# Kernel optimization log

Measured on AMD Instinct MI355X. Metric: run time of the kernel, lower is better.

Reference implementation:

```python
import jax, jax.numpy as jnp
import numpy as np

D_LATENT = 128   # per-head dim AND input embedding dim (d_q default)
N_HEADS = 16
ROPE_BASE = 10000.0


def _rope(x):
    # x: [B, H, S, D]; interleaved-pair rotary embedding over seq axis (-2)
    B, H, S, D = x.shape
    half = D // 2
    inv_freq = 1.0 / (ROPE_BASE ** (jnp.arange(half, dtype=jnp.float32) * 2.0 / D))
    ang = jnp.arange(S, dtype=jnp.float32)[:, None] * inv_freq[None, :]  # [S, half]
    cos, sin = jnp.cos(ang), jnp.sin(ang)
    xp = x.reshape(B, H, S, half, 2)
    x0, x1 = xp[..., 0], xp[..., 1]
    r0 = x0 * cos - x1 * sin
    r1 = x1 * cos + x0 * sin
    return jnp.stack([r0, r1], axis=-1).reshape(B, H, S, D)


def setup_inputs() -> dict:
    key = jax.random.key(0)
    k_q, k_wq, k_wk, k_wv, k_wo = jax.random.split(key, 5)
    B, S, E = 2, 2048, D_LATENT
    inner = N_HEADS * D_LATENT
    sc_in = 1.0 / np.sqrt(E)
    sc_inner = 1.0 / np.sqrt(inner)
    return {
        "q": jax.random.normal(k_q, (B, S, E), dtype=jnp.float32),
        "W_q": jax.random.normal(k_wq, (E, inner), dtype=jnp.float32) * sc_in,
        "W_k": jax.random.normal(k_wk, (E, inner), dtype=jnp.float32) * sc_in,
        "W_v": jax.random.normal(k_wv, (E, inner), dtype=jnp.float32) * sc_in,
        "W_o": jax.random.normal(k_wo, (inner, E), dtype=jnp.float32) * sc_inner,
    }


def reference(q, W_q, W_k, W_v, W_o):
    B, S, E = q.shape
    H, D = N_HEADS, D_LATENT
    scale = 1.0 / np.sqrt(D)
    # projections -> [B, H, S, D]
    qh = (q @ W_q).reshape(B, S, H, D).transpose(0, 2, 1, 3)
    kh = (q @ W_k).reshape(B, S, H, D).transpose(0, 2, 1, 3)
    vh = (q @ W_v).reshape(B, S, H, D).transpose(0, 2, 1, 3)
    qh = _rope(qh)
    kh = _rope(kh)
    scores = jnp.einsum("bhsd,bhtd->bhst", qh, kh) * scale  # [B,H,S,S]
    causal = jnp.tril(jnp.ones((S, S), dtype=bool))
    scores = jnp.where(causal, scores, -jnp.inf)
    probs = jax.nn.softmax(scores, axis=-1)
    out = jnp.einsum("bhst,bhtd->bhsd", probs, vh)  # [B,H,S,D]
    out = out.transpose(0, 2, 1, 3).reshape(B, S, H * D)
    return out @ W_o
```

## Files before the change

kernel.cpp:

```cpp
#include <hip/hip_runtime.h>
#include <math.h>

#define S_LEN 2048
#define NH 16
#define DH 128
#define INNER 2048
#define NROWS 4096

typedef __attribute__((ext_vector_type(8))) short bf16x8;
typedef __attribute__((ext_vector_type(4))) float f32x4;

__device__ __forceinline__ short f2bf(float f) {
  union { float f; unsigned u; } v; v.f = f;
  unsigned r = (v.u + 0x7fffu + ((v.u >> 16) & 1u)) >> 16;
  return (short)(unsigned short)r;
}
__device__ __forceinline__ float bf2f(short s) {
  union { unsigned u; float f; } v; v.u = ((unsigned)(unsigned short)s) << 16;
  return v.f;
}
__device__ __forceinline__ void gl2lds(const short* g, short* l) {
  __builtin_amdgcn_global_load_lds(
      (const __attribute__((address_space(1))) unsigned int*)g,
      (__attribute__((address_space(3))) unsigned int*)l, 16, 0, 0);
}

__global__ void k_prep(const float* __restrict__ X, const float* __restrict__ Wq,
                       const float* __restrict__ Wk, const float* __restrict__ Wv,
                       const float* __restrict__ Wo,
                       float* __restrict__ rcT, float* __restrict__ rsT,
                       short* __restrict__ Xbf, short* __restrict__ WT,
                       short* __restrict__ WoT) {
  const int bx = blockIdx.x, tid = threadIdx.x;
  if (bx < 512) {
    int idx = bx * 256 + tid;
    int i = idx >> 11, s = idx & 2047;
    double invf = pow(10000.0, -(double)i / 64.0);
    float ang = (float)((double)s * invf);
    float sv, cv; sincosf(ang, &sv, &cv);
    rcT[idx] = cv; rsT[idx] = sv;
    return;
  }
  if (bx < 1024) {
    int idx = ((bx - 512) * 256 + tid) * 4;
    float4 xv = *(const float4*)&X[idx];
    short4 o; o.x = f2bf(xv.x); o.y = f2bf(xv.y); o.z = f2bf(xv.z); o.w = f2bf(xv.w);
    *(short4*)&Xbf[idx] = o;
    return;
  }
  __shared__ float tile[32][33];
  const float* src; short* dst; int R, C, c0, r0;
  if (bx < 1792) {
    int z = (bx - 1024) >> 8, t = (bx - 1024) & 255;
    src = (z == 0) ? Wq : ((z == 1) ? Wk : Wv);
    dst = WT + (size_t)z * INNER * 128; R = 128; C = INNER;
    c0 = (t & 63) * 32; r0 = (t >> 6) * 32;
  } else {
    int t = bx - 1792;
    src = Wo; dst = WoT; R = INNER; C = 128;
    c0 = (t & 3) * 32; r0 = (t >> 2) * 32;
  }
  int tx = tid & 31, ty = tid >> 5;
  #pragma unroll
  for (int dy = 0; dy < 32; dy += 8)
    tile[ty + dy][tx] = src[(size_t)(r0 + ty + dy) * C + c0 + tx];
  __syncthreads();
  #pragma unroll
  for (int dy = 0; dy < 32; dy += 8)
    dst[(size_t)(c0 + ty + dy) * R + r0 + tx] = f2bf(tile[tx][ty + dy]);
}

__global__ __launch_bounds__(256, 2) void k_qkv(
    const short* __restrict__ Xbf, const short* __restrict__ WT,
    const float* __restrict__ rcT, const float* __restrict__ rsT,
    short* __restrict__ Qg, short* __restrict__ Kg, short* __restrict__ Vg) {
  __shared__ __attribute__((aligned(16))) short As[128 * 136];
  __shared__ __attribute__((aligned(16))) short Bs[128 * 136];
  const int tid = threadIdx.x;
  const int n0 = blockIdx.x * 128, m0 = blockIdx.y * 128;
  for (int e = tid; e < 2048; e += 256)
    *(int4*)&As[(e >> 4) * 136 + (e & 15) * 8] =
        *(const int4*)&Xbf[(size_t)(m0 + (e >> 4)) * 128 + (e & 15) * 8];
  const int wid = tid >> 6, lane = tid & 63;
  const int l16 = lane & 15, quad = lane >> 4;
  const int wm = (wid & 1) * 64, wn = (wid >> 1) * 64;
  const int hh = n0 >> 7;
  const int bb = m0 >> 11, ss = m0 & 2047;
  const float qscale = 0.08838834764831845f;
  for (int z = 0; z < 3; ++z) {
    __syncthreads();
    const short* Wp = WT + (size_t)z * INNER * 128;
    for (int e = tid; e < 2048; e += 256)
      *(int4*)&Bs[(e >> 4) * 136 + (e & 15) * 8] =
          *(const int4*)&Wp[(size_t)(n0 + (e >> 4)) * 128 + (e & 15) * 8];
    __syncthreads();
    f32x4 acc[4][4] = {};
    #pragma unroll
    for (int ks = 0; ks < 4; ++ks) {
      bf16x8 a[4], b[4];
      #pragma unroll
      for (int mt = 0; mt < 4; ++mt)
        a[mt] = *(const bf16x8*)&As[(wm + mt * 16 + l16) * 136 + ks * 32 + quad * 8];
      #pragma unroll
      for (int nt = 0; nt < 4; ++nt)
        b[nt] = *(const bf16x8*)&Bs[(wn + nt * 16 + l16) * 136 + ks * 32 + quad * 8];
      #pragma unroll
      for (int mt = 0; mt < 4; ++mt)
        #pragma unroll
        for (int nt = 0; nt < 4; ++nt)
          acc[mt][nt] = __builtin_amdgcn_mfma_f32_16x16x32_bf16(a[mt], b[nt], acc[mt][nt], 0, 0, 0);
    }
    if (z < 2) {
      __syncthreads();
      #pragma unroll
      for (int mt = 0; mt < 4; ++mt)
        #pragma unroll
        for (int nt = 0; nt < 4; ++nt) {
          int d = wn + nt * 16 + l16, i = d >> 1;
          int sl0 = wm + mt * 16 + quad * 4;
          float4 c4 = *(const float4*)&rcT[i * S_LEN + ss + sl0];
          float4 s4 = *(const float4*)&rsT[i * S_LEN + ss + sl0];
          float cA[4] = {c4.x, c4.y, c4.z, c4.w};
          float sA[4] = {s4.x, s4.y, s4.z, s4.w};
          #pragma unroll
          for (int r = 0; r < 4; ++r) {
            float v = acc[mt][nt][r];
            float pv = __shfl_xor(v, 1);
            float res = (d & 1) ? (v * cA[r] + pv * sA[r]) : (v * cA[r] - pv * sA[r]);
            if (z == 0) res *= qscale;
            Bs[(sl0 + r) * 136 + d] = f2bf(res);
          }
        }
      __syncthreads();
      short* dst = (z == 0 ? Qg : Kg) + (((size_t)(bb * NH + hh)) * S_LEN + ss) * DH;
      #pragma unroll
      for (int it = 0; it < 8; ++it) {
        int u = tid + 256 * it;
        int row = u >> 4, c = u & 15;
        int cc = (z == 0) ? c : (c ^ (row & 15));
        *(int4*)&dst[(size_t)row * DH + cc * 8] = *(const int4*)&Bs[row * 136 + c * 8];
      }
    } else {
      __syncthreads();
      #pragma unroll
      for (int mt = 0; mt < 4; ++mt)
        #pragma unroll
        for (int nt = 0; nt < 4; ++nt) {
          int dl = wn + nt * 16 + l16;
          int sl = wm + mt * 16 + quad * 4;
          short4 pk;
          pk.x = f2bf(acc[mt][nt][0]); pk.y = f2bf(acc[mt][nt][1]);
          pk.z = f2bf(acc[mt][nt][2]); pk.w = f2bf(acc[mt][nt][3]);
          *(short4*)&As[dl * 136 + sl] = pk;
        }
      __syncthreads();
      #pragma unroll
      for (int rd = 0; rd < 8; ++rd) {
        int dl = (tid >> 4) + rd * 16;
        int sl = (tid & 15) * 8;
        int tile = (ss >> 6) + (sl >> 6);
        int tl = sl & 63;
        int ch = (tl >> 3) ^ (dl & 7);
        int4 vv = *(const int4*)&As[dl * 136 + sl];
        *(int4*)&Vg[(((size_t)(bb * NH + hh) * 32 + tile) * 128 + dl) * 64 + ch * 8] = vv;
      }
    }
  }
}

__global__ __launch_bounds__(256, 2) void k_attn(
    const short* __restrict__ Qg, const short* __restrict__ Kg,
    const short* __restrict__ Vt, short* __restrict__ Op,
    float* __restrict__ mlb) {
  __shared__ __attribute__((aligned(16))) short Ks[2][64 * 128];
  __shared__ __attribute__((aligned(16))) short Vs[2][128 * 64];
  __shared__ __attribute__((aligned(16))) short Ps[4][32 * 64];
  const int bid = blockIdx.x;
  const int bh = bid & 31, unit = bid >> 5;
  const int tid = threadIdx.x, wid = tid >> 6, lane = tid & 63;
  const int l16 = lane & 15, quad = lane >> 4, wq = wid * 32;
  const float CEXP = 16.0f;
  const short* Qp = Qg + (size_t)bh * S_LEN * DH;
  const short* Kp = Kg + (size_t)bh * S_LEN * DH;
  const short* Vb = Vt + (size_t)bh * 32 * 8192;
  short* psw = &Ps[wid][0];
  int kcs[4], vcs[2];
  #pragma unroll
  for (int ks = 0; ks < 4; ++ks) kcs[ks] = ((ks * 4 + quad) ^ l16) * 8;
  #pragma unroll
  for (int ks = 0; ks < 2; ++ks) vcs[ks] = ((ks * 4 + quad) ^ (l16 & 7)) * 8;

  for (int seg = 0; seg < 2; ++seg) {
    const int qg = seg ? (15 - unit) : unit;
    const int par = seg;
    const int q0 = qg * 128, nj = qg + 1;
    __syncthreads();
    {
      const short* kg = Kp + (size_t)(par * 64) * DH;
      const short* vg = Vb + (size_t)par * 8192;
      #pragma unroll
      for (int i = 0; i < 4; ++i) {
        int sl = wid * 4 + i;
        gl2lds(kg + sl * 512 + lane * 8, &Ks[0][sl * 512]);
        gl2lds(vg + sl * 512 + lane * 8, &Vs[0][sl * 512]);
      }
    }
    bf16x8 qf[4][2];
    #pragma unroll
    for (int ks = 0; ks < 4; ++ks)
      #pragma unroll
      for (int qb = 0; qb < 2; ++qb)
        qf[ks][qb] = *(const bf16x8*)&Qp[(size_t)(q0 + wq + qb * 16 + l16) * DH +
                                         ks * 32 + quad * 8];
    float l_p[2] = {0.0f, 0.0f};
    f32x4 Oacc[8][2] = {};
    for (int jj = 0; jj < nj; ++jj) {
      const int b = jj & 1;
      __syncthreads();
      if (jj + 1 < nj) {
        const int jn = par + 2 * (jj + 1);
        const short* kg = Kp + (size_t)(jn * 64) * DH;
        const short* vg = Vb + (size_t)jn * 8192;
        #pragma unroll
        for (int i = 0; i < 4; ++i) {
          int sl = wid * 4 + i;
          gl2lds(kg + sl * 512 + lane * 8, &Ks[1 - b][sl * 512]);
          gl2lds(vg + sl * 512 + lane * 8, &Vs[1 - b][sl * 512]);
        }
      }
      f32x4 Sc[4][2] = {};
      #pragma unroll
      for (int ks = 0; ks < 4; ++ks) {
        bf16x8 kfr[4];
        #pragma unroll
        for (int nt = 0; nt < 4; ++nt)
          kfr[nt] = *(const bf16x8*)&Ks[b][(nt * 16 + l16) * 128 + kcs[ks]];
        #pragma unroll
        for (int nt = 0; nt < 4; ++nt)
          #pragma unroll
          for (int qb = 0; qb < 2; ++qb)
            Sc[nt][qb] = __builtin_amdgcn_mfma_f32_16x16x32_bf16(kfr[nt], qf[ks][qb],
                                                                 Sc[nt][qb], 0, 0, 0);
      }
      const int j = par + 2 * jj;
      if (jj == nj - 1) {
        #pragma unroll
        for (int nt = 0; nt < 4; ++nt)
          #pragma unroll
          for (int qb = 0; qb < 2; ++qb)
            #pragma unroll
            for (int r = 0; r < 4; ++r) {
              int tg = j * 64 + nt * 16 + quad * 4 + r;
              int qgl = q0 + wq + qb * 16 + l16;
              if (tg > qgl) Sc[nt][qb][r] = -60.0f;
            }
      }
      #pragma unroll
      for (int qb = 0; qb < 2; ++qb) {
        float ls = 0.0f;
        #pragma unroll
        for (int nt = 0; nt < 4; ++nt)
          #pragma unroll
          for (int r = 0; r < 4; ++r) {
            float pe = __expf(Sc[nt][qb][r] - CEXP);
            Sc[nt][qb][r] = pe;
            ls += pe;
          }
        l_p[qb] += ls;
        #pragma unroll
        for (int nt = 0; nt < 4; ++nt) {
          short4 pk;
          pk.x = f2bf(Sc[nt][qb][0]); pk.y = f2bf(Sc[nt][qb][1]);
          pk.z = f2bf(Sc[nt][qb][2]); pk.w = f2bf(Sc[nt][qb][3]);
          int ch = ((nt * 2 + (quad >> 1)) ^ (l16 & 7)) * 8 + (quad & 1) * 4;
          *(short4*)&psw[(qb * 16 + l16) * 64 + ch] = pk;
        }
      }
      #pragma unroll
      for (int ks = 0; ks < 2; ++ks) {
        bf16x8 vfr[8];
        #pragma unroll
        for (int nt = 0; nt < 8; ++nt)
          vfr[nt] = *(const bf16x8*)&Vs[b][(nt * 16 + l16) * 64 + vcs[ks]];
        bf16x8 bp[2];
        #pragma unroll
        for (int qb = 0; qb < 2; ++qb)
          bp[qb] = *(const bf16x8*)&psw[(qb * 16 + l16) * 64 + vcs[ks]];
        #pragma unroll
        for (int nt = 0; nt < 8; ++nt)
          #pragma unroll
          for (int qb = 0; qb < 2; ++qb)
            Oacc[nt][qb] = __builtin_amdgcn_mfma_f32_16x16x32_bf16(vfr[nt], bp[qb],
                                                                   Oacc[nt][qb], 0, 0, 0);
      }
    }
    __syncthreads();
    short* osl = &Ks[0][0] + wid * 4096;
    #pragma unroll
    for (int qb = 0; qb < 2; ++qb)
      #pragma unroll
      for (int nt = 0; nt < 8; ++nt) {
        short4 ov;
        ov.x = f2bf(Oacc[nt][qb][0]); ov.y = f2bf(Oacc[nt][qb][1]);
        ov.z = f2bf(Oacc[nt][qb][2]); ov.w = f2bf(Oacc[nt][qb][3]);
        int ch = ((nt * 2 + (quad >> 1)) ^ l16) * 8 + (quad & 1) * 4;
        *(short4*)&osl[(qb * 16 + l16) * 128 + ch] = ov;
      }
    size_t obase = ((size_t)(par * 32 + bh) * S_LEN + q0 + wq) * DH;
    #pragma unroll
    for (int it = 0; it < 8; ++it) {
      int u = lane + 64 * it;
      int row = u >> 4, c = u & 15;
      *(int4*)&Op[obase + (size_t)row * DH + c * 8] =
          *(const int4*)&osl[row * 128 + ((c ^ (row & 15)) * 8)];
    }
    #pragma unroll
    for (int qb = 0; qb < 2; ++qb) {
      float lt = l_p[qb];
      lt += __shfl_xor(lt, 16);
      lt += __shfl_xor(lt, 32);
      int qrow = q0 + wq + qb * 16 + l16;
      if (quad == 0)
        mlb[(size_t)(par * 32 + bh) * S_LEN + qrow] = lt;
    }
  }
}

__global__ __launch_bounds__(256) void k_out(
    const short* __restrict__ Op, const float* __restrict__ mlb,
    const short* __restrict__ WoT, float* __restrict__ out) {
  __shared__ __attribute__((aligned(16))) short As[32 * 72];
  __shared__ __attribute__((aligned(16))) short Bs[128 * 72];
  __shared__ float cw[8][32];
  const int m0 = blockIdx.x * 32, kb0 = blockIdx.y * 1024;
  const int tid = threadIdx.x, wid = tid >> 6, lane = tid & 63;
  const int l16 = lane & 15, quad = lane >> 4;
  const int wm = (wid & 1) * 16, wn = (wid >> 1) * 64;
  {
    int rr = tid & 31, hh = tid >> 5;
    int row = m0 + rr, b = row >> 11, s = row & 2047;
    int bh = b * NH + (kb0 >> 7) + hh;
    float l1 = mlb[(size_t)bh * S_LEN + s];
    float l2 = mlb[(size_t)(32 + bh) * S_LEN + s];
    cw[hh][rr] = 1.0f / (l1 + l2);
  }
  __syncthreads();
  f32x4 acc[4] = {};
  for (int kc = 0; kc < 16; ++kc) {
    int k0 = kb0 + kc * 64;
    int h = k0 >> 7, d0 = k0 & 127, hh = kc >> 1;
    #pragma unroll
    for (int it = 0; it < 2; ++it) {
      int e = tid + 256 * it;
      int rr = e >> 4, c4 = (e & 15) * 4;
      int row = m0 + rr, b = row >> 11, s = row & 2047;
      size_t base = ((size_t)(b * NH + h) * S_LEN + s) * DH + d0 + c4;
      short4 u1 = *(const short4*)&Op[base];
      short4 u2 = *(const short4*)&Op[(size_t)32 * S_LEN * DH + base];
      float c1 = cw[hh][rr];
      short4 o;
      o.x = f2bf(c1 * (bf2f(u1.x) + bf2f(u2.x)));
      o.y = f2bf(c1 * (bf2f(u1.y) + bf2f(u2.y)));
      o.z = f2bf(c1 * (bf2f(u1.z) + bf2f(u2.z)));
      o.w = f2bf(c1 * (bf2f(u1.w) + bf2f(u2.w)));
      *(short4*)&As[rr * 72 + c4] = o;
    }
    for (int e = tid; e < 1024; e += 256)
      *(int4*)&Bs[(e >> 3) * 72 + (e & 7) * 8] =
          *(const int4*)&WoT[(size_t)(e >> 3) * INNER + k0 + (e & 7) * 8];
    __syncthreads();
    #pragma unroll
    for (int ks = 0; ks < 2; ++ks) {
      bf16x8 a = *(const bf16x8*)&As[(wm + l16) * 72 + ks * 32 + quad * 8];
      bf16x8 b[4];
      #pragma unroll
      for (int nt = 0; nt < 4; ++nt)
        b[nt] = *(const bf16x8*)&Bs[(wn + nt * 16 + l16) * 72 + ks * 32 + quad * 8];
      #pragma unroll
      for (int nt = 0; nt < 4; ++nt)
        acc[nt] = __builtin_amdgcn_mfma_f32_16x16x32_bf16(a, b[nt], acc[nt], 0, 0, 0);
    }
    __syncthreads();
  }
  #pragma unroll
  for (int nt = 0; nt < 4; ++nt)
    #pragma unroll
    for (int r = 0; r < 4; ++r) {
      int gm = m0 + wm + quad * 4 + r;
      int gn = wn + nt * 16 + l16;
      atomicAdd(&out[(size_t)gm * 128 + gn], acc[nt][r]);
    }
}

extern "C" void kernel_launch(void* const* d_in, const int* in_sizes, int n_in,
                              void* d_out, int out_size, void* d_ws, size_t ws_size,
                              hipStream_t stream) {
  const float* q  = (const float*)d_in[0];
  const float* Wq = (const float*)d_in[1];
  const float* Wk = (const float*)d_in[2];
  const float* Wv = (const float*)d_in[3];
  const float* Wo = (const float*)d_in[4];
  float* out = (float*)d_out;
  char* ws = (char*)d_ws;
  const size_t MB = 1024 * 1024;
  float* rcT = (float*)(ws + 0);
  float* rsT = (float*)(ws + 512 * 1024);
  short* WT  = (short*)(ws + 1 * MB);
  short* WoT = (short*)(ws + 2 * MB + 512 * 1024);
  short* Xbf = (short*)(ws + 3 * MB);
  short* Qg  = (short*)(ws + 8 * MB);
  short* Kg  = (short*)(ws + 24 * MB);
  short* Vg  = (short*)(ws + 40 * MB);
  short* Op  = (short*)(ws + 56 * MB);
  float* mlb = (float*)(ws + 88 * MB);

  k_prep<<<2048, 256, 0, stream>>>(q, Wq, Wk, Wv, Wo, rcT, rsT, Xbf, WT, WoT);
  k_qkv<<<dim3(16, 32), 256, 0, stream>>>(Xbf, WT, rcT, rsT, Qg, Kg, Vg);
  k_attn<<<512, 256, 0, stream>>>(Qg, Kg, Vg, Op, mlb);
  hipMemsetAsync(d_out, 0, (size_t)out_size * sizeof(float), stream);
  k_out<<<dim3(128, 2), 256, 0, stream>>>(Op, mlb, WoT, out);
}
```

Measured before the change: 181.5 us.

## Fold output zeroing into prep, interleave rope table, transpose QK MFMA, retile out-proj

The output memset moves into extra blocks of the prep kernel, which removes one launch. The rope cos/sin tables are interleaved per position so each lane loads one float4 holding a pair's cos and sin. The Q/K MFMAs are computed transposed so each lane holds adjacent head-dim pairs, which removes the shuffles in the rope epilogue and lets results go out as packed short4. The output projection is retiled to one 128-wide head per k-step, with four head groups per row block and two blocks per CU, at the cost of more atomic adds into the output.

```diff
diff --git a/kernel.cpp b/kernel.cpp
--- a/kernel.cpp
+++ b/kernel.cpp
@@ -28,17 +28,17 @@
 __global__ void k_prep(const float* __restrict__ X, const float* __restrict__ Wq,
                        const float* __restrict__ Wk, const float* __restrict__ Wv,
                        const float* __restrict__ Wo,
-                       float* __restrict__ rcT, float* __restrict__ rsT,
-                       short* __restrict__ Xbf, short* __restrict__ WT,
-                       short* __restrict__ WoT) {
+                       float* __restrict__ csT, short* __restrict__ Xbf,
+                       short* __restrict__ WT, short* __restrict__ WoT,
+                       float* __restrict__ outz) {
   const int bx = blockIdx.x, tid = threadIdx.x;
   if (bx < 512) {
     int idx = bx * 256 + tid;
-    int i = idx >> 11, s = idx & 2047;
+    int i = idx & 63, s = idx >> 6;
     double invf = pow(10000.0, -(double)i / 64.0);
     float ang = (float)((double)s * invf);
     float sv, cv; sincosf(ang, &sv, &cv);
-    rcT[idx] = cv; rsT[idx] = sv;
+    csT[idx * 2] = cv; csT[idx * 2 + 1] = sv;
     return;
   }
   if (bx < 1024) {
@@ -46,6 +46,12 @@
     float4 xv = *(const float4*)&X[idx];
     short4 o; o.x = f2bf(xv.x); o.y = f2bf(xv.y); o.z = f2bf(xv.z); o.w = f2bf(xv.w);
     *(short4*)&Xbf[idx] = o;
+    return;
+  }
+  if (bx >= 2048) {
+    float4 z4 = make_float4(0.f, 0.f, 0.f, 0.f);
+    ((float4*)outz)[(bx - 2048) * 512 + tid] = z4;
+    ((float4*)outz)[(bx - 2048) * 512 + tid + 256] = z4;
     return;
   }
   __shared__ float tile[32][33];
@@ -72,7 +78,7 @@
 
 __global__ __launch_bounds__(256, 2) void k_qkv(
     const short* __restrict__ Xbf, const short* __restrict__ WT,
-    const float* __restrict__ rcT, const float* __restrict__ rsT,
+    const float* __restrict__ csT,
     short* __restrict__ Qg, short* __restrict__ Kg, short* __restrict__ Vg) {
   __shared__ __attribute__((aligned(16))) short As[128 * 136];
   __shared__ __attribute__((aligned(16))) short Bs[128 * 136];
@@ -97,39 +103,44 @@
     f32x4 acc[4][4] = {};
     #pragma unroll
     for (int ks = 0; ks < 4; ++ks) {
-      bf16x8 a[4], b[4];
-      #pragma unroll
-      for (int mt = 0; mt < 4; ++mt)
-        a[mt] = *(const bf16x8*)&As[(wm + mt * 16 + l16) * 136 + ks * 32 + quad * 8];
-      #pragma unroll
-      for (int nt = 0; nt < 4; ++nt)
-        b[nt] = *(const bf16x8*)&Bs[(wn + nt * 16 + l16) * 136 + ks * 32 + quad * 8];
-      #pragma unroll
-      for (int mt = 0; mt < 4; ++mt)
-        #pragma unroll
-        for (int nt = 0; nt < 4; ++nt)
-          acc[mt][nt] = __builtin_amdgcn_mfma_f32_16x16x32_bf16(a[mt], b[nt], acc[mt][nt], 0, 0, 0);
+      bf16x8 ax[4], bw[4];
+      #pragma unroll
+      for (int j = 0; j < 4; ++j) {
+        ax[j] = *(const bf16x8*)&As[(wm + j * 16 + l16) * 136 + ks * 32 + quad * 8];
+        bw[j] = *(const bf16x8*)&Bs[(wn + j * 16 + l16) * 136 + ks * 32 + quad * 8];
+      }
+      if (z < 2) {
+        #pragma unroll
+        for (int dt = 0; dt < 4; ++dt)
+          #pragma unroll
+          for (int st = 0; st < 4; ++st)
+            acc[dt][st] = __builtin_amdgcn_mfma_f32_16x16x32_bf16(bw[dt], ax[st], acc[dt][st], 0, 0, 0);
+      } else {
+        #pragma unroll
+        for (int mt = 0; mt < 4; ++mt)
+          #pragma unroll
+          for (int nt = 0; nt < 4; ++nt)
+            acc[mt][nt] = __builtin_amdgcn_mfma_f32_16x16x32_bf16(ax[mt], bw[nt], acc[mt][nt], 0, 0, 0);
+      }
     }
     if (z < 2) {
       __syncthreads();
       #pragma unroll
-      for (int mt = 0; mt < 4; ++mt)
-        #pragma unroll
-        for (int nt = 0; nt < 4; ++nt) {
-          int d = wn + nt * 16 + l16, i = d >> 1;
-          int sl0 = wm + mt * 16 + quad * 4;
-          float4 c4 = *(const float4*)&rcT[i * S_LEN + ss + sl0];
-          float4 s4 = *(const float4*)&rsT[i * S_LEN + ss + sl0];
-          float cA[4] = {c4.x, c4.y, c4.z, c4.w};
-          float sA[4] = {s4.x, s4.y, s4.z, s4.w};
-          #pragma unroll
-          for (int r = 0; r < 4; ++r) {
-            float v = acc[mt][nt][r];
-            float pv = __shfl_xor(v, 1);
-            float res = (d & 1) ? (v * cA[r] + pv * sA[r]) : (v * cA[r] - pv * sA[r]);
-            if (z == 0) res *= qscale;
-            Bs[(sl0 + r) * 136 + d] = f2bf(res);
-          }
+      for (int dt = 0; dt < 4; ++dt)
+        #pragma unroll
+        for (int st = 0; st < 4; ++st) {
+          int d0 = wn + dt * 16 + quad * 4;
+          int sl = wm + st * 16 + l16;
+          int sg = ss + sl;
+          float4 cs = *(const float4*)&csT[((size_t)sg * 64 + (d0 >> 1)) * 2];
+          float x0 = acc[dt][st][0], x1 = acc[dt][st][1];
+          float x2 = acc[dt][st][2], x3 = acc[dt][st][3];
+          float r0 = x0 * cs.x - x1 * cs.y, r1 = x1 * cs.x + x0 * cs.y;
+          float r2 = x2 * cs.z - x3 * cs.w, r3 = x3 * cs.z + x2 * cs.w;
+          if (z == 0) { r0 *= qscale; r1 *= qscale; r2 *= qscale; r3 *= qscale; }
+          short4 pk;
+          pk.x = f2bf(r0); pk.y = f2bf(r1); pk.z = f2bf(r2); pk.w = f2bf(r3);
+          *(short4*)&Bs[sl * 136 + d0] = pk;
         }
       __syncthreads();
       short* dst = (z == 0 ? Qg : Kg) + (((size_t)(bb * NH + hh)) * S_LEN + ss) * DH;
@@ -326,56 +337,55 @@
   }
 }
 
-__global__ __launch_bounds__(256) void k_out(
+__global__ __launch_bounds__(256, 2) void k_out(
     const short* __restrict__ Op, const float* __restrict__ mlb,
     const short* __restrict__ WoT, float* __restrict__ out) {
-  __shared__ __attribute__((aligned(16))) short As[32 * 72];
-  __shared__ __attribute__((aligned(16))) short Bs[128 * 72];
-  __shared__ float cw[8][32];
-  const int m0 = blockIdx.x * 32, kb0 = blockIdx.y * 1024;
+  __shared__ __attribute__((aligned(16))) short As[32 * 136];
+  __shared__ __attribute__((aligned(16))) short Bs[128 * 136];
+  __shared__ float cw[4][32];
+  const int m0 = blockIdx.x * 32, h0 = blockIdx.y * 4;
   const int tid = threadIdx.x, wid = tid >> 6, lane = tid & 63;
   const int l16 = lane & 15, quad = lane >> 4;
   const int wm = (wid & 1) * 16, wn = (wid >> 1) * 64;
-  {
+  if (tid < 128) {
     int rr = tid & 31, hh = tid >> 5;
     int row = m0 + rr, b = row >> 11, s = row & 2047;
-    int bh = b * NH + (kb0 >> 7) + hh;
+    int bh = b * NH + h0 + hh;
     float l1 = mlb[(size_t)bh * S_LEN + s];
     float l2 = mlb[(size_t)(32 + bh) * S_LEN + s];
     cw[hh][rr] = 1.0f / (l1 + l2);
   }
   __syncthreads();
   f32x4 acc[4] = {};
-  for (int kc = 0; kc < 16; ++kc) {
-    int k0 = kb0 + kc * 64;
-    int h = k0 >> 7, d0 = k0 & 127, hh = kc >> 1;
-    #pragma unroll
-    for (int it = 0; it < 2; ++it) {
+  for (int hc = 0; hc < 4; ++hc) {
+    int h = h0 + hc;
+    #pragma unroll
+    for (int it = 0; it < 4; ++it) {
       int e = tid + 256 * it;
-      int rr = e >> 4, c4 = (e & 15) * 4;
+      int rr = e >> 5, c4 = (e & 31) * 4;
       int row = m0 + rr, b = row >> 11, s = row & 2047;
-      size_t base = ((size_t)(b * NH + h) * S_LEN + s) * DH + d0 + c4;
+      size_t base = ((size_t)(b * NH + h) * S_LEN + s) * DH + c4;
       short4 u1 = *(const short4*)&Op[base];
       short4 u2 = *(const short4*)&Op[(size_t)32 * S_LEN * DH + base];
-      float c1 = cw[hh][rr];
+      float c1 = cw[hc][rr];
       short4 o;
       o.x = f2bf(c1 * (bf2f(u1.x) + bf2f(u2.x)));
       o.y = f2bf(c1 * (bf2f(u1.y) + bf2f(u2.y)));
       o.z = f2bf(c1 * (bf2f(u1.z) + bf2f(u2.z)));
       o.w = f2bf(c1 * (bf2f(u1.w) + bf2f(u2.w)));
-      *(short4*)&As[rr * 72 + c4] = o;
-    }
-    for (int e = tid; e < 1024; e += 256)
-      *(int4*)&Bs[(e >> 3) * 72 + (e & 7) * 8] =
-          *(const int4*)&WoT[(size_t)(e >> 3) * INNER + k0 + (e & 7) * 8];
-    __syncthreads();
-    #pragma unroll
-    for (int ks = 0; ks < 2; ++ks) {
-      bf16x8 a = *(const bf16x8*)&As[(wm + l16) * 72 + ks * 32 + quad * 8];
+      *(short4*)&As[rr * 136 + c4] = o;
+    }
+    for (int e = tid; e < 2048; e += 256)
+      *(int4*)&Bs[(e >> 4) * 136 + (e & 15) * 8] =
+          *(const int4*)&WoT[(size_t)(e >> 4) * INNER + h * 128 + (e & 15) * 8];
+    __syncthreads();
+    #pragma unroll
+    for (int ks = 0; ks < 4; ++ks) {
+      bf16x8 a = *(const bf16x8*)&As[(wm + l16) * 136 + ks * 32 + quad * 8];
       bf16x8 b[4];
       #pragma unroll
       for (int nt = 0; nt < 4; ++nt)
-        b[nt] = *(const bf16x8*)&Bs[(wn + nt * 16 + l16) * 72 + ks * 32 + quad * 8];
+        b[nt] = *(const bf16x8*)&Bs[(wn + nt * 16 + l16) * 136 + ks * 32 + quad * 8];
       #pragma unroll
       for (int nt = 0; nt < 4; ++nt)
         acc[nt] = __builtin_amdgcn_mfma_f32_16x16x32_bf16(a, b[nt], acc[nt], 0, 0, 0);
@@ -403,8 +413,7 @@
   float* out = (float*)d_out;
   char* ws = (char*)d_ws;
   const size_t MB = 1024 * 1024;
-  float* rcT = (float*)(ws + 0);
-  float* rsT = (float*)(ws + 512 * 1024);
+  float* csT = (float*)(ws + 0);
   short* WT  = (short*)(ws + 1 * MB);
   short* WoT = (short*)(ws + 2 * MB + 512 * 1024);
   short* Xbf = (short*)(ws + 3 * MB);
@@ -414,9 +423,8 @@
   short* Op  = (short*)(ws + 56 * MB);
   float* mlb = (float*)(ws + 88 * MB);
 
-  k_prep<<<2048, 256, 0, stream>>>(q, Wq, Wk, Wv, Wo, rcT, rsT, Xbf, WT, WoT);
-  k_qkv<<<dim3(16, 32), 256, 0, stream>>>(Xbf, WT, rcT, rsT, Qg, Kg, Vg);
+  k_prep<<<2304, 256, 0, stream>>>(q, Wq, Wk, Wv, Wo, csT, Xbf, WT, WoT, out);
+  k_qkv<<<dim3(16, 32), 256, 0, stream>>>(Xbf, WT, csT, Qg, Kg, Vg);
   k_attn<<<512, 256, 0, stream>>>(Qg, Kg, Vg, Op, mlb);
-  hipMemsetAsync(d_out, 0, (size_t)out_size * sizeof(float), stream);
-  k_out<<<dim3(128, 2), 256, 0, stream>>>(Op, mlb, WoT, out);
-}
+  k_out<<<dim3(128, 4), 256, 0, stream>>>(Op, mlb, WoT, out);
+}
```

Result: faster. 159.3 us (-12.3%).
